# Kernel optimization log

Hardware: AMD Instinct MI355X
Metric: run time of the kernel (lower is better)

## Reference

```python
import jax, jax.numpy as jnp
import numpy as np

B, S, D, H, HD = 4, 2048, 1024, 16, 64


def setup_inputs() -> dict:
    key = jax.random.key(0)
    k1, k2, k3 = jax.random.split(key, 3)
    x = jax.random.normal(k1, (B, S, D), dtype=jnp.float32)
    w_attn = jax.random.normal(k2, (D, 3, H, HD), dtype=jnp.float32) * 0.02
    b_attn = jnp.zeros((3, H, HD), dtype=jnp.float32)
    w_proj = jax.random.normal(k3, (H, HD, D), dtype=jnp.float32) * 0.02
    b_proj = jnp.zeros((D,), dtype=jnp.float32)
    return {"x": x, "w_attn": w_attn, "b_attn": b_attn, "w_proj": w_proj, "b_proj": b_proj}


def reference(x, w_attn, b_attn, w_proj, b_proj):
    # c_attn: [B,S,D] x [D,3,H,HD] -> [B,3,H,S,HD]
    qkv = jnp.einsum('bsd,dqhe->bqhse', x, w_attn) + b_attn[None, :, :, None, :]
    q, k, v = qkv[:, 0], qkv[:, 1], qkv[:, 2]  # each [B,H,S,HD]
    scale = 1.0 / jnp.sqrt(jnp.asarray(HD, dtype=q.dtype))
    scores = jnp.einsum('bhse,bhte->bhst', q * scale, k)  # [B,H,S,S]
    causal = jnp.tril(jnp.ones((S, S), dtype=bool))
    scores = jnp.where(causal, scores, jnp.asarray(-1e9, dtype=scores.dtype))
    attn = jax.nn.softmax(scores, axis=-1)
    out = jnp.einsum('bhst,bhte->bhse', attn, v)  # [B,H,S,HD]
    # c_proj: contract (heads, head_size) -> embed
    return jnp.einsum('bhse,hed->bsd', out, w_proj) + b_proj
```

## Files before the change

### kernel.cpp

```cpp
#include <hip/hip_runtime.h>

#define NB 4
#define NS 2048
#define ND 1024
#define NH 16
#define NE 64
#define NM (NB*NS)

typedef __attribute__((ext_vector_type(8))) __bf16 bf16x8;
typedef __attribute__((ext_vector_type(4))) float f32x4;

__device__ __forceinline__ float bf2f(unsigned short h) {
  union { unsigned u; float f; } c; c.u = ((unsigned)h) << 16; return c.f;
}
__device__ __forceinline__ unsigned short f2bf(float f) {
  union { float f; unsigned u; } c; c.f = f;
  return (unsigned short)((c.u + 0x7fffu + ((c.u >> 16) & 1u)) >> 16);
}
__device__ __forceinline__ void load16_to_lds(const void* g, void* l) {
  __builtin_amdgcn_global_load_lds(
      (__attribute__((address_space(1))) void*)(void*)(unsigned long long)(const char*)g,
      (__attribute__((address_space(3))) void*)l, 16, 0, 0);
}

__global__ void detect_dtype(const unsigned* __restrict__ x, int* __restrict__ flag) {
  __shared__ int cnt;
  if (threadIdx.x == 0) cnt = 0;
  __syncthreads();
  unsigned w = x[((unsigned)threadIdx.x * 16381u) & ((1u << 21) - 1u)];
  unsigned lo = w & 0xFFFFu;
  int e = (int)((lo >> 7) & 0xFF);
  int plausible = (lo == 0u) || (e >= 100 && e <= 142);
  atomicAdd(&cnt, plausible);
  __syncthreads();
  if (threadIdx.x == 0) *flag = (cnt >= 192) ? 1 : 0;
}

__global__ void conv_to_bf16(const void* __restrict__ src, unsigned short* __restrict__ dst,
                             int n, const int* __restrict__ flag) {
  int stride = gridDim.x * blockDim.x;
  int i0 = blockIdx.x * blockDim.x + threadIdx.x;
  if (*flag) {
    const unsigned short* s = (const unsigned short*)src;
    for (int i = i0; i < n; i += stride) dst[i] = s[i];
  } else {
    const float* s = (const float*)src;
    for (int i = i0; i < n; i += stride) dst[i] = f2bf(s[i]);
  }
}

__global__ __launch_bounds__(256) void transpose_conv(const void* __restrict__ in,
                                                      unsigned short* __restrict__ out,
                                                      int K, int N, const int* __restrict__ flag) {
  __shared__ unsigned short tile[32][33];
  int n0 = blockIdx.x * 32, k0 = blockIdx.y * 32;
  int tx = threadIdx.x, ty = threadIdx.y;
  if (*flag) {
    const unsigned short* p = (const unsigned short*)in;
#pragma unroll
    for (int i = 0; i < 4; ++i)
      tile[ty + 8*i][tx] = p[(size_t)(k0 + ty + 8*i) * N + n0 + tx];
  } else {
    const float* p = (const float*)in;
#pragma unroll
    for (int i = 0; i < 4; ++i)
      tile[ty + 8*i][tx] = f2bf(p[(size_t)(k0 + ty + 8*i) * N + n0 + tx]);
  }
  __syncthreads();
#pragma unroll
  for (int i = 0; i < 4; ++i)
    out[(size_t)(n0 + ty + 8*i) * K + k0 + tx] = tile[tx][ty + 8*i];
}

#define BUFB 49152

__device__ __forceinline__ void gemm_core_v5(const unsigned short* __restrict__ Ag,
                                             const unsigned short* __restrict__ Btg,
                                             int m0, int n0,
                                             unsigned short* sm,
                                             f32x4 (&acc)[4][4]) {
  char* smb = (char*)sm;
  const int t = threadIdx.x;
  const int lane = t & 63, w = t >> 6;
  const int wr = w >> 1, wc = w & 1;
  const int frm = lane & 15, qd = lane >> 4;
  const int px0 = ((qd    ) ^ (frm & 7)) * 16;
  const int px1 = ((4 + qd) ^ (frm & 7)) * 16;
  const int NT = ND / 64;

  auto stage = [&](int kt, int b) {
    char* Ab = smb + b * BUFB;
    char* Bb = Ab + 32768;
    int kk = kt * 64;
#pragma unroll
    for (int u = 0; u < 4; ++u) {
      int ci = u * 512 + t;
      int row = ci >> 3, c = ci & 7, l = c ^ (row & 7);
      load16_to_lds(Ag + (size_t)(m0 + row) * ND + kk + l * 8, Ab + ci * 16);
    }
#pragma unroll
    for (int u = 0; u < 2; ++u) {
      int ci = u * 512 + t;
      int row = ci >> 3, c = ci & 7, l = c ^ (row & 7);
      load16_to_lds(Btg + (size_t)(n0 + row) * ND + kk + l * 8, Bb + ci * 16);
    }
  };

  stage(0, 0);
  asm volatile("s_waitcnt vmcnt(0)\n\ts_barrier" ::: "memory");

  for (int kt = 0; kt < NT; ++kt) {
    const int cur = kt & 1;
    const char* Ab = smb + cur * BUFB;
    const char* Bb = Ab + 32768;

    if (kt + 1 < NT) stage(kt + 1, cur ^ 1);

    bf16x8 a[4][2], b[4][2];
#pragma unroll
    for (int i = 0; i < 4; ++i) {
      int row = 64*wr + 16*i + frm;
      a[i][0] = *(const bf16x8*)(Ab + row * 128 + px0);
      a[i][1] = *(const bf16x8*)(Ab + row * 128 + px1);
    }
#pragma unroll
    for (int j = 0; j < 4; ++j) {
      int row = 64*wc + 16*j + frm;
      b[j][0] = *(const bf16x8*)(Bb + row * 128 + px0);
      b[j][1] = *(const bf16x8*)(Bb + row * 128 + px1);
    }
    asm volatile("s_waitcnt lgkmcnt(0)" ::: "memory");
    __builtin_amdgcn_s_setprio(1);
#pragma unroll
    for (int i = 0; i < 4; ++i)
#pragma unroll
      for (int j = 0; j < 4; ++j) {
        acc[i][j] = __builtin_amdgcn_mfma_f32_16x16x32_bf16(a[i][0], b[j][0], acc[i][j], 0, 0, 0);
        acc[i][j] = __builtin_amdgcn_mfma_f32_16x16x32_bf16(a[i][1], b[j][1], acc[i][j], 0, 0, 0);
      }
    __builtin_amdgcn_s_setprio(0);
    if (kt + 1 < NT)
      asm volatile("s_waitcnt vmcnt(0)\n\ts_barrier" ::: "memory");
  }
}

__global__ __launch_bounds__(512, 2) void gemm_qkv_v5(const unsigned short* __restrict__ X,
                                                      const unsigned short* __restrict__ W1T,
                                                      const unsigned short* __restrict__ battn,
                                                      unsigned short* __restrict__ qb,
                                                      unsigned short* __restrict__ kb,
                                                      unsigned short* __restrict__ vb) {
  __shared__ unsigned short sm[2 * 384 * 64];
  int flat = blockIdx.x + 24 * blockIdx.y;
  int virt = (flat & 7) * 96 + (flat >> 3);
  const int n0 = (virt % 24) * 128;
  const int m0 = (virt / 24) * 256;

  f32x4 acc[4][4] = {};
  gemm_core_v5(X, W1T, m0, n0, sm, acc);

  const int t = threadIdx.x, lane = t & 63, w = t >> 6;
  const int wr = w >> 1, wc = w & 1;
  const int coln = lane & 15, rbase = (lane >> 4) * 4;
#pragma unroll
  for (int j = 0; j < 4; ++j) {
    int nn = n0 + 64*wc + 16*j + coln;
    int qq = nn >> 10;
    int h  = (nn >> 6) & 15;
    int e  = nn & 63;
    float bias = bf2f(battn[nn]);
    float scale = (qq == 0) ? (0.125f * 1.44269504f) : 1.0f;
    if (qq == 2) {
#pragma unroll
      for (int i = 0; i < 4; ++i) {
        int mm0 = m0 + 64*wr + 16*i + rbase;
        int bb = mm0 >> 11, s0 = mm0 & 2047;
        unsigned long long pk = 0;
#pragma unroll
        for (int rr = 0; rr < 4; ++rr) {
          float v = acc[i][j][rr] + bias;
          pk |= ((unsigned long long)f2bf(v)) << (16 * rr);
        }
        size_t idx = (((size_t)bb * NH + h) * NE + e) * NS + s0;
        *(unsigned long long*)(vb + idx) = pk;
      }
    } else {
      unsigned short* dst = (qq == 0) ? qb : kb;
#pragma unroll
      for (int i = 0; i < 4; ++i) {
#pragma unroll
        for (int rr = 0; rr < 4; ++rr) {
          int mm = m0 + 64*wr + 16*i + rbase + rr;
          int bb = mm >> 11, s = mm & 2047;
          float v = (acc[i][j][rr] + bias) * scale;
          dst[(((size_t)bb * NH + h) * NS + s) * NE + e] = f2bf(v);
        }
      }
    }
  }
}

__global__ __launch_bounds__(512, 2) void gemm_proj_v5(const unsigned short* __restrict__ A,
                                                       const unsigned short* __restrict__ W2T,
                                                       const unsigned short* __restrict__ bproj,
                                                       void* __restrict__ outv,
                                                       const int* __restrict__ flag) {
  __shared__ unsigned short sm[2 * 384 * 64];
  int flat = blockIdx.x + 8 * blockIdx.y;
  int virt = (flat & 7) * 32 + (flat >> 3);
  const int n0 = (virt % 8) * 128;
  const int m0 = (virt / 8) * 256;

  f32x4 acc[4][4] = {};
  gemm_core_v5(A, W2T, m0, n0, sm, acc);

  const int isbf = *flag;
  unsigned short* out16 = (unsigned short*)outv;
  float* out32 = (float*)outv;
  const int t = threadIdx.x, lane = t & 63, w = t >> 6;
  const int wr = w >> 1, wc = w & 1;
  const int coln = lane & 15, rbase = (lane >> 4) * 4;
#pragma unroll
  for (int j = 0; j < 4; ++j) {
    int nn = n0 + 64*wc + 16*j + coln;
    float bias = bf2f(bproj[nn]);
#pragma unroll
    for (int i = 0; i < 4; ++i) {
#pragma unroll
      for (int rr = 0; rr < 4; ++rr) {
        int mm = m0 + 64*wr + 16*i + rbase + rr;
        float v = acc[i][j][rr] + bias;
        if (isbf) out16[(size_t)mm * ND + nn] = f2bf(v);
        else      out32[(size_t)mm * ND + nn] = v;
      }
    }
  }
}

__global__ __launch_bounds__(256, 4) void attn_causal(const unsigned short* __restrict__ qb,
                                                      const unsigned short* __restrict__ kb,
                                                      const unsigned short* __restrict__ vtb,
                                                      unsigned short* __restrict__ ob) {
  __shared__ unsigned short QPs[128 * 64];
  __shared__ unsigned short Ks[2][32 * 64];
  __shared__ unsigned short Vt[2][32 * 64];

  int t = threadIdx.x, lane = t & 63, w = t >> 6;
  int qd = lane >> 4, li = lane & 15;
  int sw0 = ((qd ^ (li & 7)) * 8);
  int sw1 = (((4 + qd) ^ (li & 7)) * 8);

  const int qtab[4][4] = {{15,8,7,0},{14,9,6,1},{13,10,5,2},{12,11,4,3}};
  int bi = blockIdx.x;
  int bh = bi & 63;
  int qt = qtab[(bi >> 6) & 3][bi >> 8];
  int q0 = qt * 128;
  int NT = 4 * qt + 4;
  size_t base = (size_t)bh * NS * NE;
  int bb = bh >> 4, hh = bh & 15;

  bf16x8 onesf;
#pragma unroll
  for (int j = 0; j < 8; ++j) onesf[j] = (__bf16)1.0f;

  unsigned pofs[2][2][4];
#pragma unroll
  for (int i = 0; i < 2; ++i)
#pragma unroll
    for (int c = 0; c < 2; ++c)
#pragma unroll
      for (int rr = 0; rr < 4; ++rr) {
        int prow = 32*w + 16*i + qd*4 + rr;
        int lo = 2*c + (li >> 3);
        pofs[i][c][rr] = (unsigned)((prow * 64 + ((lo ^ (prow & 7)) * 8) + (li & 7)) * 2);
        asm volatile("" : "+v"(pofs[i][c][rr]));
      }

  {
  }
  int r8 = t >> 3, p8 = t & 7, lsw = p8 ^ (r8 & 7);
  const char* ksrc = (const char*)(kb + base + (size_t)r8 * NE + lsw * 8);
  int ve = 2 * r8 + (lsw >> 2);
  const char* vsrc = (const char*)(vtb + base + (size_t)ve * NS + (lsw & 3) * 8);
  char* kdst = (char*)Ks[0] + t * 16;
  char* vdst = (char*)Vt[0] + t * 16;

  auto stage_kv = [&](int buf) {
    load16_to_lds(ksrc, kdst + buf * 4096);
    load16_to_lds(vsrc, vdst + buf * 4096);
    ksrc += 32 * NE * 2;
    vsrc += 32 * 2;
  };

#pragma unroll
  for (int c = 0; c < 4; ++c) {
    int ch = c * 256 + t;
    int r = ch >> 3, jl = (ch & 7) ^ (r & 7);
    load16_to_lds(qb + base + (size_t)(q0 + r) * NE + jl * 8, (char*)QPs + ch * 16);
  }
  stage_kv(0);
  asm volatile("s_waitcnt vmcnt(2)\n\ts_barrier" ::: "memory");

  bf16x8 qa[2][2];
#pragma unroll
  for (int i = 0; i < 2; ++i) {
    const unsigned short* qr = QPs + (32*w + 16*i + li) * 64;
    qa[i][0] = *(const bf16x8*)(qr + sw0);
    qa[i][1] = *(const bf16x8*)(qr + sw1);
  }

  f32x4 o[2][4] = {};
  f32x4 lacc[2] = {};

  for (int kt = 0; kt < NT; ++kt) {
    int cur = kt & 1;
    asm volatile("s_waitcnt lgkmcnt(0)\n\ts_barrier" ::: "memory");
    if (kt + 1 < NT) {
      stage_kv(cur ^ 1);
      asm volatile("s_waitcnt vmcnt(2)\n\ts_barrier" ::: "memory");
    } else {
      asm volatile("s_waitcnt vmcnt(0)\n\ts_barrier" ::: "memory");
    }

    int k0 = kt * 32;
    const unsigned short* Ksc = Ks[cur];
    const unsigned short* Vtc = Vt[cur];

    bf16x8 kfr[2][2];
#pragma unroll
    for (int c = 0; c < 2; ++c) {
      const unsigned short* kr = Ksc + (16*c + li) * 64;
      kfr[c][0] = *(const bf16x8*)(kr + sw0);
      kfr[c][1] = *(const bf16x8*)(kr + sw1);
    }

    int need_mask = (k0 >= q0);
#pragma unroll
    for (int i = 0; i < 2; ++i) {
#pragma unroll
      for (int c = 0; c < 2; ++c) {
        f32x4 s = {};
        s = __builtin_amdgcn_mfma_f32_16x16x32_bf16(qa[i][0], kfr[c][0], s, 0, 0, 0);
        s = __builtin_amdgcn_mfma_f32_16x16x32_bf16(qa[i][1], kfr[c][1], s, 0, 0, 0);
#pragma unroll
        for (int rr = 0; rr < 4; ++rr) {
          float pv = exp2f(s[rr]);
          if (need_mask) {
            int colk = k0 + 16*c + li;
            int rowq = q0 + 32*w + 16*i + qd*4 + rr;
            if (colk > rowq) pv = 0.f;
          }
          *(unsigned short*)((char*)QPs + pofs[i][c][rr]) =
              (unsigned short)(__float_as_uint(pv) >> 16);
        }
      }
    }

    bf16x8 pa[2];
#pragma unroll
    for (int i = 0; i < 2; ++i)
      pa[i] = *(const bf16x8*)(QPs + (32*w + 16*i + li) * 64 + sw0);

#pragma unroll
    for (int i = 0; i < 2; ++i)
      lacc[i] = __builtin_amdgcn_mfma_f32_16x16x32_bf16(pa[i], onesf, lacc[i], 0, 0, 0);

#pragma unroll
    for (int c2 = 0; c2 < 4; ++c2) {
      const unsigned short* vr = Vtc + (8*c2 + (li >> 1)) * 64;
      bf16x8 vf = *(const bf16x8*)(vr + ((((li & 1) * 4 + qd) ^ ((li >> 1) & 7)) * 8));
#pragma unroll
      for (int i = 0; i < 2; ++i)
        o[i][c2] = __builtin_amdgcn_mfma_f32_16x16x32_bf16(pa[i], vf, o[i][c2], 0, 0, 0);
    }
  }

#pragma unroll
  for (int i = 0; i < 2; ++i)
#pragma unroll
    for (int c = 0; c < 4; ++c)
#pragma unroll
      for (int rr = 0; rr < 4; ++rr) {
        int rowm = 32*w + 16*i + qd*4 + rr;
        float inv = 1.0f / fmaxf(lacc[i][rr], 1e-30f);
        float ov = o[i][c][rr] * inv;
        int e = 16*c + li;
        ob[(((size_t)bb * NS + (q0 + rowm)) * NH + hh) * NE + e] = f2bf(ov);
      }
}

extern "C" void kernel_launch(void* const* d_in, const int* in_sizes, int n_in,
                              void* d_out, int out_size, void* d_ws, size_t ws_size,
                              hipStream_t stream) {
  (void)in_sizes; (void)n_in; (void)out_size; (void)ws_size;
  char* ws = (char*)d_ws;
  unsigned short* W1T = (unsigned short*)(ws);
  unsigned short* W2T = (unsigned short*)(ws + 6291456);
  unsigned short* qb  = (unsigned short*)(ws + 8388608);
  unsigned short* kb  = (unsigned short*)(ws + 25165824);
  unsigned short* vb  = (unsigned short*)(ws + 41943040);
  unsigned short* ob  = (unsigned short*)(ws + 58720256);
  unsigned short* bac = (unsigned short*)(ws + 75497472);
  unsigned short* bpc = (unsigned short*)(ws + 75505664);
  int*            flg = (int*)(ws + 75513856);
  unsigned short* xc  = ob;

  detect_dtype<<<1, 256, 0, stream>>>((const unsigned*)d_in[0], flg);
  conv_to_bf16<<<2048, 256, 0, stream>>>(d_in[0], xc,  NB*NS*ND, flg);
  conv_to_bf16<<<12,   256, 0, stream>>>(d_in[2], bac, 3*NH*NE, flg);
  conv_to_bf16<<<4,    256, 0, stream>>>(d_in[4], bpc, ND, flg);

  transpose_conv<<<dim3(3072/32, 1024/32), dim3(32, 8), 0, stream>>>(d_in[1], W1T, 1024, 3072, flg);
  transpose_conv<<<dim3(1024/32, 1024/32), dim3(32, 8), 0, stream>>>(d_in[3], W2T, 1024, 1024, flg);
  gemm_qkv_v5<<<dim3(3072/128, NM/256), 512, 0, stream>>>(xc, W1T, bac, qb, kb, vb);
  attn_causal<<<dim3(1024), 256, 0, stream>>>(qb, kb, vb, ob);
  gemm_proj_v5<<<dim3(1024/128, NM/256), 512, 0, stream>>>(ob, W2T, bpc, d_out, flg);
}
```

Measured before the change: 262.5 us.

## Pair complementary 64-row causal query chunks per attention block for load balance

Each attention block now handles two 64-row query chunks, c0 and 31-c0, in sequence instead of one 128-row tile picked through a lookup table. Every block therefore does a near-equal amount of causal work, and the smaller Q/P tile halves that shared buffer. In exchange each warp covers 16 query rows instead of 32, so every K/V tile loaded is reused by fewer rows. K/V tiles are reloaded for the second chunk, and the chunks run serially inside a block.

```diff
diff --git a/kernel.cpp b/kernel.cpp
--- a/kernel.cpp
+++ b/kernel.cpp
@@ -241,7 +241,7 @@
                                                       const unsigned short* __restrict__ kb,
                                                       const unsigned short* __restrict__ vtb,
                                                       unsigned short* __restrict__ ob) {
-  __shared__ unsigned short QPs[128 * 64];
+  __shared__ unsigned short QPs[64 * 64];
   __shared__ unsigned short Ks[2][32 * 64];
   __shared__ unsigned short Vt[2][32 * 64];
 
@@ -250,12 +250,9 @@
   int sw0 = ((qd ^ (li & 7)) * 8);
   int sw1 = (((4 + qd) ^ (li & 7)) * 8);
 
-  const int qtab[4][4] = {{15,8,7,0},{14,9,6,1},{13,10,5,2},{12,11,4,3}};
   int bi = blockIdx.x;
   int bh = bi & 63;
-  int qt = qtab[(bi >> 6) & 3][bi >> 8];
-  int q0 = qt * 128;
-  int NT = 4 * qt + 4;
+  int c0 = bi >> 6;
   size_t base = (size_t)bh * NS * NE;
   int bb = bh >> 4, hh = bh & 15;
 
@@ -263,130 +260,122 @@
 #pragma unroll
   for (int j = 0; j < 8; ++j) onesf[j] = (__bf16)1.0f;
 
-  unsigned pofs[2][2][4];
-#pragma unroll
-  for (int i = 0; i < 2; ++i)
-#pragma unroll
-    for (int c = 0; c < 2; ++c)
-#pragma unroll
-      for (int rr = 0; rr < 4; ++rr) {
-        int prow = 32*w + 16*i + qd*4 + rr;
-        int lo = 2*c + (li >> 3);
-        pofs[i][c][rr] = (unsigned)((prow * 64 + ((lo ^ (prow & 7)) * 8) + (li & 7)) * 2);
-        asm volatile("" : "+v"(pofs[i][c][rr]));
-      }
-
-  {
-  }
+  unsigned pofs[2][4];
+#pragma unroll
+  for (int c = 0; c < 2; ++c)
+#pragma unroll
+    for (int rr = 0; rr < 4; ++rr) {
+      int prow = 16*w + qd*4 + rr;
+      int lo = 2*c + (li >> 3);
+      pofs[c][rr] = (unsigned)((prow * 64 + ((lo ^ (prow & 7)) * 8) + (li & 7)) * 2);
+    }
+
   int r8 = t >> 3, p8 = t & 7, lsw = p8 ^ (r8 & 7);
-  const char* ksrc = (const char*)(kb + base + (size_t)r8 * NE + lsw * 8);
+  const char* ksrc0 = (const char*)(kb + base + (size_t)r8 * NE + lsw * 8);
   int ve = 2 * r8 + (lsw >> 2);
-  const char* vsrc = (const char*)(vtb + base + (size_t)ve * NS + (lsw & 3) * 8);
+  const char* vsrc0 = (const char*)(vtb + base + (size_t)ve * NS + (lsw & 3) * 8);
   char* kdst = (char*)Ks[0] + t * 16;
   char* vdst = (char*)Vt[0] + t * 16;
 
-  auto stage_kv = [&](int buf) {
-    load16_to_lds(ksrc, kdst + buf * 4096);
-    load16_to_lds(vsrc, vdst + buf * 4096);
-    ksrc += 32 * NE * 2;
-    vsrc += 32 * 2;
-  };
-
-#pragma unroll
-  for (int c = 0; c < 4; ++c) {
-    int ch = c * 256 + t;
-    int r = ch >> 3, jl = (ch & 7) ^ (r & 7);
-    load16_to_lds(qb + base + (size_t)(q0 + r) * NE + jl * 8, (char*)QPs + ch * 16);
-  }
-  stage_kv(0);
-  asm volatile("s_waitcnt vmcnt(2)\n\ts_barrier" ::: "memory");
-
-  bf16x8 qa[2][2];
-#pragma unroll
-  for (int i = 0; i < 2; ++i) {
-    const unsigned short* qr = QPs + (32*w + 16*i + li) * 64;
-    qa[i][0] = *(const bf16x8*)(qr + sw0);
-    qa[i][1] = *(const bf16x8*)(qr + sw1);
-  }
-
-  f32x4 o[2][4] = {};
-  f32x4 lacc[2] = {};
-
-  for (int kt = 0; kt < NT; ++kt) {
-    int cur = kt & 1;
-    asm volatile("s_waitcnt lgkmcnt(0)\n\ts_barrier" ::: "memory");
-    if (kt + 1 < NT) {
-      stage_kv(cur ^ 1);
-      asm volatile("s_waitcnt vmcnt(2)\n\ts_barrier" ::: "memory");
-    } else {
-      asm volatile("s_waitcnt vmcnt(0)\n\ts_barrier" ::: "memory");
-    }
-
-    int k0 = kt * 32;
-    const unsigned short* Ksc = Ks[cur];
-    const unsigned short* Vtc = Vt[cur];
-
-    bf16x8 kfr[2][2];
-#pragma unroll
-    for (int c = 0; c < 2; ++c) {
-      const unsigned short* kr = Ksc + (16*c + li) * 64;
-      kfr[c][0] = *(const bf16x8*)(kr + sw0);
-      kfr[c][1] = *(const bf16x8*)(kr + sw1);
-    }
-
-    int need_mask = (k0 >= q0);
-#pragma unroll
-    for (int i = 0; i < 2; ++i) {
+#pragma unroll 1
+  for (int half = 0; half < 2; ++half) {
+    const int qc = half ? (31 - c0) : c0;
+    const int q0 = qc * 64;
+    const int NT = 2 * qc + 2;
+
+    if (half) {
+      asm volatile("s_waitcnt lgkmcnt(0)\n\ts_barrier" ::: "memory");
+    }
+
+#pragma unroll
+    for (int cc = 0; cc < 2; ++cc) {
+      int ch = cc * 256 + t;
+      int r = ch >> 3, jl = (ch & 7) ^ (r & 7);
+      load16_to_lds(qb + base + (size_t)(q0 + r) * NE + jl * 8, (char*)QPs + ch * 16);
+    }
+    const char* ksrc = ksrc0;
+    const char* vsrc = vsrc0;
+    load16_to_lds(ksrc, kdst);
+    load16_to_lds(vsrc, vdst);
+    ksrc += 32 * NE * 2;  vsrc += 32 * 2;
+    asm volatile("s_waitcnt vmcnt(2)\n\ts_barrier" ::: "memory");
+
+    bf16x8 qa0, qa1;
+    {
+      const unsigned short* qr = QPs + (16*w + li) * 64;
+      qa0 = *(const bf16x8*)(qr + sw0);
+      qa1 = *(const bf16x8*)(qr + sw1);
+    }
+
+    f32x4 o[4] = {};
+    f32x4 lacc = {};
+
+    for (int kt = 0; kt < NT; ++kt) {
+      int cur = kt & 1;
+      asm volatile("s_waitcnt lgkmcnt(0)\n\ts_barrier" ::: "memory");
+      if (kt + 1 < NT) {
+        load16_to_lds(ksrc, kdst + (cur ^ 1) * 4096);
+        load16_to_lds(vsrc, vdst + (cur ^ 1) * 4096);
+        ksrc += 32 * NE * 2;  vsrc += 32 * 2;
+        asm volatile("s_waitcnt vmcnt(2)\n\ts_barrier" ::: "memory");
+      } else {
+        asm volatile("s_waitcnt vmcnt(0)\n\ts_barrier" ::: "memory");
+      }
+
+      int k0 = kt * 32;
+      const unsigned short* Ksc = Ks[cur];
+      const unsigned short* Vtc = Vt[cur];
+
+      bf16x8 kfr[2][2];
+#pragma unroll
+      for (int c = 0; c < 2; ++c) {
+        const unsigned short* kr = Ksc + (16*c + li) * 64;
+        kfr[c][0] = *(const bf16x8*)(kr + sw0);
+        kfr[c][1] = *(const bf16x8*)(kr + sw1);
+      }
+
+      int need_mask = (k0 >= q0);
 #pragma unroll
       for (int c = 0; c < 2; ++c) {
         f32x4 s = {};
-        s = __builtin_amdgcn_mfma_f32_16x16x32_bf16(qa[i][0], kfr[c][0], s, 0, 0, 0);
-        s = __builtin_amdgcn_mfma_f32_16x16x32_bf16(qa[i][1], kfr[c][1], s, 0, 0, 0);
+        s = __builtin_amdgcn_mfma_f32_16x16x32_bf16(qa0, kfr[c][0], s, 0, 0, 0);
+        s = __builtin_amdgcn_mfma_f32_16x16x32_bf16(qa1, kfr[c][1], s, 0, 0, 0);
 #pragma unroll
         for (int rr = 0; rr < 4; ++rr) {
           float pv = exp2f(s[rr]);
           if (need_mask) {
             int colk = k0 + 16*c + li;
-            int rowq = q0 + 32*w + 16*i + qd*4 + rr;
+            int rowq = q0 + 16*w + qd*4 + rr;
             if (colk > rowq) pv = 0.f;
           }
-          *(unsigned short*)((char*)QPs + pofs[i][c][rr]) =
+          *(unsigned short*)((char*)QPs + pofs[c][rr]) =
               (unsigned short)(__float_as_uint(pv) >> 16);
         }
       }
-    }
-
-    bf16x8 pa[2];
-#pragma unroll
-    for (int i = 0; i < 2; ++i)
-      pa[i] = *(const bf16x8*)(QPs + (32*w + 16*i + li) * 64 + sw0);
-
-#pragma unroll
-    for (int i = 0; i < 2; ++i)
-      lacc[i] = __builtin_amdgcn_mfma_f32_16x16x32_bf16(pa[i], onesf, lacc[i], 0, 0, 0);
-
-#pragma unroll
-    for (int c2 = 0; c2 < 4; ++c2) {
-      const unsigned short* vr = Vtc + (8*c2 + (li >> 1)) * 64;
-      bf16x8 vf = *(const bf16x8*)(vr + ((((li & 1) * 4 + qd) ^ ((li >> 1) & 7)) * 8));
-#pragma unroll
-      for (int i = 0; i < 2; ++i)
-        o[i][c2] = __builtin_amdgcn_mfma_f32_16x16x32_bf16(pa[i], vf, o[i][c2], 0, 0, 0);
-    }
-  }
-
-#pragma unroll
-  for (int i = 0; i < 2; ++i)
-#pragma unroll
-    for (int c = 0; c < 4; ++c)
+
+      bf16x8 pa = *(const bf16x8*)(QPs + (16*w + li) * 64 + sw0);
+
+      lacc = __builtin_amdgcn_mfma_f32_16x16x32_bf16(pa, onesf, lacc, 0, 0, 0);
+
+#pragma unroll
+      for (int c2 = 0; c2 < 4; ++c2) {
+        const unsigned short* vr = Vtc + (8*c2 + (li >> 1)) * 64;
+        bf16x8 vf = *(const bf16x8*)(vr + ((((li & 1) * 4 + qd) ^ ((li >> 1) & 7)) * 8));
+        o[c2] = __builtin_amdgcn_mfma_f32_16x16x32_bf16(pa, vf, o[c2], 0, 0, 0);
+      }
+    }
+
+#pragma unroll
+    for (int c2 = 0; c2 < 4; ++c2)
 #pragma unroll
       for (int rr = 0; rr < 4; ++rr) {
-        int rowm = 32*w + 16*i + qd*4 + rr;
-        float inv = 1.0f / fmaxf(lacc[i][rr], 1e-30f);
-        float ov = o[i][c][rr] * inv;
-        int e = 16*c + li;
+        int rowm = 16*w + qd*4 + rr;
+        float inv = 1.0f / fmaxf(lacc[rr], 1e-30f);
+        float ov = o[c2][rr] * inv;
+        int e = 16*c2 + li;
         ob[(((size_t)bb * NS + (q0 + rowm)) * NH + hh) * NE + e] = f2bf(ov);
       }
+  }
 }
 
 extern "C" void kernel_launch(void* const* d_in, const int* in_sizes, int n_in,
```

Measured after the change: 270.1 us. +2.9%, slower.
